# Kernel tuning notes

Hardware: AMD Instinct MI355X
Metric: run time of the kernel (lower is better)

## Reference

```python
import jax, jax.numpy as jnp
import numpy as np

B, T, V, D = 64, 2048, 32000, 256  # batch, seq_len, vocab, emb_dim == hidden_size
H = D
NUM_CLASSES = 27
N_NODES = 128


def setup_inputs() -> dict:
    key = jax.random.key(0)
    ks = jax.random.split(key, 8)
    s = 1.0 / np.sqrt(D)
    return {
        "tokens": jax.random.randint(ks[0], (B, T), 0, V),
        "node_token_span_starts": jax.random.randint(ks[1], (B, N_NODES), 0, T),
        "node_token_span_ends": jax.random.randint(ks[2], (B, N_NODES), 0, T),
        "embed": jax.random.normal(ks[3], (V, D), dtype=jnp.float32),
        "Wi": jax.random.normal(ks[4], (D, 4 * H), dtype=jnp.float32) * s,
        "Wh": jax.random.normal(ks[5], (H, 4 * H), dtype=jnp.float32) * s,
        "bh": jnp.zeros((4 * H,), dtype=jnp.float32),
        "Wo": jax.random.normal(ks[6], (H, NUM_CLASSES), dtype=jnp.float32) * s,
        "bo": jnp.zeros((NUM_CLASSES,), dtype=jnp.float32),
    }


def reference(tokens, node_token_span_starts, node_token_span_ends,
              embed, Wi, Wh, bh, Wo, bo):
    # node_token_span_* are unused by the original forward (dead code).
    x = embed[tokens.astype(jnp.int32)]            # [B, T, D]
    # Precompute input projections for all timesteps in one big GEMM.
    zx = jnp.einsum('btd,df->btf', x, Wi) + bh     # [B, T, 4H]
    batch = tokens.shape[0]
    c0 = jnp.zeros((batch, H), dtype=x.dtype)
    h0 = jnp.zeros((batch, H), dtype=x.dtype)

    def step(carry, zxt):
        c, h = carry
        z = zxt + h @ Wh                           # [B, 4H]
        i, f, g, o = jnp.split(z, 4, axis=-1)
        c = jax.nn.sigmoid(f) * c + jax.nn.sigmoid(i) * jnp.tanh(g)
        h = jax.nn.sigmoid(o) * jnp.tanh(c)
        return (c, h), h

    (c, h), _ = jax.lax.scan(step, (c0, h0), jnp.swapaxes(zx, 0, 1))
    # forward_outputs[:, -1, :] == final hidden state h
    return h @ Wo + bo                             # [B, NUM_CLASSES]
```

## Files before the change

### kernel.cpp

```cpp
#include <hip/hip_runtime.h>
#include <hip/hip_bf16.h>
#include <stdint.h>

typedef __hip_bfloat16 bf16;
typedef __attribute__((ext_vector_type(8))) short short8;
typedef __attribute__((ext_vector_type(4))) float f32x4;
typedef __attribute__((ext_vector_type(4))) int i32x4;
typedef __attribute__((ext_vector_type(4))) unsigned int u32x4;

#define NB   64
#define NT   2048
#define NV   32000
#define ND   256
#define NH4  1024
#define NCLS 27
#define CH   256
#define NCH  (NT / CH)


__global__ __launch_bounds__(256) void k_cvt_embed(const float* __restrict__ e,
                                                   bf16* __restrict__ o) {
  int i = blockIdx.x * blockDim.x + threadIdx.x;
  float4 v = reinterpret_cast<const float4*>(e)[i];
  union { bf16 h[4]; uint2 u; } pk;
  pk.h[0] = __float2bfloat16(v.x);
  pk.h[1] = __float2bfloat16(v.y);
  pk.h[2] = __float2bfloat16(v.z);
  pk.h[3] = __float2bfloat16(v.w);
  reinterpret_cast<uint2*>(o)[i] = pk.u;
}

__global__ __launch_bounds__(256) void k_cvt_wi(const float* __restrict__ wi,
                                                bf16* __restrict__ wit) {
  int i = blockIdx.x * blockDim.x + threadIdx.x;
  int col = i >> 8;
  int k   = i & 255;
  wit[i] = __float2bfloat16(wi[k * NH4 + col]);
}

__global__ __launch_bounds__(256) void k_scale(const float* __restrict__ wh,
                                               float* __restrict__ dq,
                                               float* __restrict__ rdq,
                                               float* __restrict__ rw) {
  int col = blockIdx.x * 256 + threadIdx.x;
  float m = 0.f;
  for (int k = 0; k < ND; ++k) m = fmaxf(m, fabsf(wh[k * NH4 + col]));
  dq[col]  = m * (1.f / 16129.f);
  rdq[col] = 16129.f / m;
  rw[col]  = 127.f / m;
}

__global__ __launch_bounds__(256) void k_cvt_whq(const float* __restrict__ wh,
                                                 const float* __restrict__ rw,
                                                 signed char* __restrict__ whq) {
  int idx  = blockIdx.x * 256 + threadIdx.x;
  int ii   = idx & 15;
  int lane = (idx >> 4) & 63;
  int kq   = (idx >> 10) & 3;
  int nt   = idx >> 12;
  int k   = kq * 64 + (lane >> 4) * 16 + ii;
  int col = nt * 16 + (lane & 15);
  whq[idx] = (signed char)(int)rintf(wh[k * NH4 + col] * rw[col]);
}

__device__ __forceinline__ float sigf(float x) {
  return __builtin_amdgcn_rcpf(1.f + __expf(-x));
}
__device__ __forceinline__ float tanh_fast(float x) {
  return 1.f - 2.f * __builtin_amdgcn_rcpf(1.f + __expf(2.f * x));
}

#define LSTM_STEP(ZX, ST)                                                       \
  {                                                                             \
    i32x4 a0 = *(const i32x4*)&aF[0 * 1024 + l * 16];                           \
    i32x4 a1 = *(const i32x4*)&aF[1 * 1024 + l * 16];                           \
    i32x4 a2 = *(const i32x4*)&aF[2 * 1024 + l * 16];                           \
    i32x4 a3 = *(const i32x4*)&aF[3 * 1024 + l * 16];                           \
    i32x4 acc[8];                                                               \
    _Pragma("unroll")                                                           \
    for (int j = 0; j < 8; ++j) {                                               \
      i32x4 t;                                                                  \
      t = __builtin_amdgcn_mfma_i32_16x16x64_i8(a0, w[j][0], czero, 0, 0, 0);   \
      t = __builtin_amdgcn_mfma_i32_16x16x64_i8(a1, w[j][1], t, 0, 0, 0);       \
      t = __builtin_amdgcn_mfma_i32_16x16x64_i8(a2, w[j][2], t, 0, 0, 0);       \
      acc[j] = __builtin_amdgcn_mfma_i32_16x16x64_i8(a3, w[j][3], t, 0, 0, 0);  \
    }                                                                           \
    if (l4 == 0) {                                                              \
      _Pragma("unroll")                                                         \
      for (int j = 0; j < 8; ++j) {                                             \
        int col = (wv * 8 + j) * 16 + l15;                                      \
        int tt  = ((col & 255) << 2) | (col >> 8);                              \
        zl[tt]        = acc[j][0];                                              \
        zl[1024 + tt] = acc[j][1];                                              \
      }                                                                         \
    }                                                                           \
    __syncthreads();                                                            \
    {                                                                           \
      i32x4 zr = *(const i32x4*)&zl[b * 1024 + u * 4];                          \
      int s0 = zr[0] + ZX[0];                                                   \
      int s1 = zr[1] + ZX[1];                                                   \
      int s2 = zr[2] + ZX[2];                                                   \
      int s3 = zr[3] + ZX[3];                                                   \
      if ((ST) + 2 < CH)                                                        \
        ZX = *(const i32x4*)(zg + (size_t)((ST) + 2) * 2048);                   \
      float zi = (float)s0 * dqv[0] + bhv[0];                                   \
      float zf = (float)s1 * dqv[1] + bhv[1];                                   \
      float zg_ = (float)s2 * dqv[2] + bhv[2];                                  \
      float zo = (float)s3 * dqv[3] + bhv[3];                                   \
      c = sigf(zf) * c + sigf(zi) * tanh_fast(zg_);                             \
      float h = sigf(zo) * tanh_fast(c);                                        \
      aF[kqu * 1024 + (b | (lgu << 4)) * 16 + iiu] =                            \
          (signed char)(int)rintf(h * 127.f);                                   \
      if ((ST) == CH - 1) hst[(p * 2 + b) * 256 + u] = h;                       \
    }                                                                           \
    __syncthreads();                                                            \
  }

__global__ __launch_bounds__(512, 1) void k_fused(const int*  __restrict__ tokens,
                                                  const bf16* __restrict__ eb,
                                                  const bf16* __restrict__ wit,
                                                  const float* __restrict__ rdq,
                                                  const signed char* __restrict__ whq,
                                                  const float* __restrict__ dq,
                                                  const float* __restrict__ bh,
                                                  float* __restrict__ cst,
                                                  float* __restrict__ hst,
                                                  int* __restrict__ zxqA,
                                                  int* __restrict__ zxqB,
                                                  int L) {
  __shared__ char smem[16384];
  int bid = blockIdx.x;

  if (bid < 32) {
    if (L == 0) return;
    int* zl = (int*)smem;
    signed char* aF = (signed char*)(smem + 8192);
    const int* __restrict__ zxq = ((L - 1) & 1) ? zxqB : zxqA;
    int t0 = (L - 1) * CH;

    int p   = bid;
    int tid = threadIdx.x;
    int l   = tid & 63;
    int wv  = tid >> 6;
    int l15 = l & 15, l4 = l >> 4;
    int u   = tid & 255;
    int b   = tid >> 8;

    i32x4 w[8][4];
#pragma unroll
    for (int j = 0; j < 8; ++j) {
      int nt = wv * 8 + j;
#pragma unroll
      for (int kq = 0; kq < 4; ++kq)
        w[j][kq] = *(const i32x4*)&whq[((nt * 4 + kq) * 64 + l) * 16];
    }
#pragma unroll
    for (int j = 0; j < 8; ++j)
#pragma unroll
      for (int kq = 0; kq < 4; ++kq)
        asm volatile("" : "+v"(w[j][kq]));

    i32x4 czero = (i32x4)0;
    asm volatile("" : "+v"(czero));

    float dqv[4], bhv[4];
#pragma unroll
    for (int q = 0; q < 4; ++q) { dqv[q] = dq[q * 256 + u]; bhv[q] = bh[q * 256 + u]; }
    float c = (t0 == 0) ? 0.f : cst[(p * 2 + b) * 256 + u];

    int kqu = u >> 6, lgu = (u >> 4) & 3, iiu = u & 15;

    if (tid < 256) ((i32x4*)aF)[tid] = (i32x4)0;
    __syncthreads();
    if (t0 != 0) {
      int hq = (int)rintf(hst[(p * 2 + b) * 256 + u] * 127.f);
      aF[kqu * 1024 + (b | (lgu << 4)) * 16 + iiu] = (signed char)hq;
    }
    __syncthreads();

    const int* zg = zxq + ((size_t)(p * CH) * 2 + b) * 1024 + u * 4;
    i32x4 zxA = *(const i32x4*)zg;
    i32x4 zxB = *(const i32x4*)(zg + 2048);

    for (int lt = 0; lt < CH; lt += 2) {
      LSTM_STEP(zxA, lt)
      LSTM_STEP(zxB, lt + 1)
    }

    cst[(p * 2 + b) * 256 + u] = c;

  } else {
    if (L >= NCH) return;
    int* __restrict__ zxw = (L & 1) ? zxqB : zxqA;
    int t0 = L * CH;
    int hh   = threadIdx.x >> 8;
    int tid2 = threadIdx.x & 255;
    bf16* As = (bf16*)(smem + hh * 8192);
    bf16* Bs = (bf16*)(smem + hh * 8192 + 4096);

    int lane = tid2 & 63, wave = tid2 >> 6;
    int wm   = wave >> 1, wn = wave & 1;
    int srow = tid2 >> 2;
    int skg  = tid2 & 3;
    bf16* as_dst = &As[(skg * 64 + srow) * 8];
    bf16* bs_dst = &Bs[(skg * 64 + srow) * 8];

    for (int it = 0; it < 16; ++it) {
      int tg = ((bid - 32) + it * 128) * 2 + hh;
      int mb = tg >> 4;
      int nb = tg & 15;
      int n0 = nb * 64;

      long trow = (long)tokens[srow * NT + t0 + mb] * ND;
      const bf16* ap = eb  + trow + skg * 8;
      const bf16* bp = wit + (long)(n0 + srow) * ND + skg * 8;

      f32x4 acc[2][2] = {};
      for (int k0 = 0; k0 < ND; k0 += 32) {
        __syncthreads();
        *(u32x4*)as_dst = *(const u32x4*)(ap + k0);
        *(u32x4*)bs_dst = *(const u32x4*)(bp + k0);
        __syncthreads();
        short8 a0 = *(const short8*)&As[((lane >> 4) * 64 + wm * 32 +  0 + (lane & 15)) * 8];
        short8 a1 = *(const short8*)&As[((lane >> 4) * 64 + wm * 32 + 16 + (lane & 15)) * 8];
        short8 b0 = *(const short8*)&Bs[((lane >> 4) * 64 + wn * 32 +  0 + (lane & 15)) * 8];
        short8 b1 = *(const short8*)&Bs[((lane >> 4) * 64 + wn * 32 + 16 + (lane & 15)) * 8];
        acc[0][0] = __builtin_amdgcn_mfma_f32_16x16x32_bf16(a0, b0, acc[0][0], 0, 0, 0);
        acc[0][1] = __builtin_amdgcn_mfma_f32_16x16x32_bf16(a0, b1, acc[0][1], 0, 0, 0);
        acc[1][0] = __builtin_amdgcn_mfma_f32_16x16x32_bf16(a1, b0, acc[1][0], 0, 0, 0);
        acc[1][1] = __builtin_amdgcn_mfma_f32_16x16x32_bf16(a1, b1, acc[1][1], 0, 0, 0);
      }

      int cb  = n0 + wn * 32 + (lane & 15);
      float rq0 = rdq[cb], rq1 = rdq[cb + 16];
      int bb = wm * 32 + (lane >> 4) * 4;
#pragma unroll
      for (int fm = 0; fm < 2; ++fm) {
#pragma unroll
        for (int fn = 0; fn < 2; ++fn) {
          int col = cb + fn * 16;
          int uu  = col & 255, q = col >> 8;
          float rq = fn ? rq1 : rq0;
#pragma unroll
          for (int i2 = 0; i2 < 4; ++i2) {
            int rr = bb + fm * 16 + i2;
            int p0 = rr >> 1;
            size_t idx = (((size_t)(p0 * CH) + mb) * 2 + (rr & 1)) * 1024 + uu * 4 + q;
            zxw[idx] = (int)rintf(acc[fm][fn][i2] * rq);
          }
        }
      }
    }
  }
}

__global__ __launch_bounds__(64) void k_out(const float* __restrict__ hfin,
                                            const float* __restrict__ wo,
                                            const float* __restrict__ bo,
                                            float* __restrict__ y) {
  __shared__ float hsm[256];
  int b = blockIdx.x, tid = threadIdx.x;
  for (int i = tid; i < 256; i += 64) hsm[i] = hfin[b * 256 + i];
  __syncthreads();
  if (tid < NCLS) {
    float s = bo[tid];
    for (int k = 0; k < 256; ++k) s += hsm[k] * wo[k * NCLS + tid];
    y[b * NCLS + tid] = s;
  }
}

extern "C" void kernel_launch(void* const* d_in, const int* in_sizes, int n_in,
                              void* d_out, int out_size, void* d_ws, size_t ws_size,
                              hipStream_t stream) {
  const int*   tokens = (const int*)d_in[0];
  const float* embed  = (const float*)d_in[3];
  const float* wi     = (const float*)d_in[4];
  const float* wh     = (const float*)d_in[5];
  const float* bh     = (const float*)d_in[6];
  const float* wo     = (const float*)d_in[7];
  const float* bo     = (const float*)d_in[8];
  float* y = (float*)d_out;

  char* ws = (char*)d_ws;
  bf16* eb         = (bf16*)ws;        ws += (size_t)NV * ND * 2;
  bf16* wit        = (bf16*)ws;        ws += (size_t)NH4 * ND * 2;
  signed char* whq = (signed char*)ws; ws += (size_t)ND * NH4;
  float* dqv       = (float*)ws;       ws += (size_t)NH4 * 4;
  float* rdq       = (float*)ws;       ws += (size_t)NH4 * 4;
  float* rw        = (float*)ws;       ws += (size_t)NH4 * 4;
  float* cst       = (float*)ws;       ws += (size_t)NB * ND * 4;
  float* hst       = (float*)ws;       ws += (size_t)NB * ND * 4;
  int* zxqA        = (int*)ws;         ws += (size_t)CH * 262144;
  int* zxqB        = (int*)ws;         ws += (size_t)CH * 262144;

  hipLaunchKernelGGL(k_cvt_embed, dim3(NV * ND / 4 / 256), dim3(256), 0, stream, embed, eb);
  hipLaunchKernelGGL(k_cvt_wi,    dim3(NH4 * ND / 256), dim3(256), 0, stream, wi, wit);
  hipLaunchKernelGGL(k_scale,     dim3(4), dim3(256), 0, stream, wh, dqv, rdq, rw);
  hipLaunchKernelGGL(k_cvt_whq,   dim3(1024), dim3(256), 0, stream, wh, rw, whq);

  for (int L = 0; L <= NCH; ++L) {
    hipLaunchKernelGGL(k_fused, dim3(160), dim3(512), 0, stream,
                       tokens, eb, wit, rdq, whq, dqv, bh, cst, hst,
                       zxqA, zxqB, L);
  }
  hipLaunchKernelGGL(k_out, dim3(NB), dim3(64), 0, stream, hst, wo, bo, y);
}
```

Baseline: 2.161 ms.

## Compute LSTM gates directly from MFMA accumulators with double-buffered h

Remaps the recurrent weight tiles so each wave's MFMA outputs hold all four gates for the same hidden units, so gate math runs in registers on the accumulator lanes. This removes the shared-memory z staging buffer and one of the two barriers per timestep, and double-buffers the quantized h fragment. The cost is that only a quarter of the lanes (l4==0) do the nonlinearities, four units each, which concentrates transcendental work on fewer threads.

```diff
diff --git a/kernel.cpp b/kernel.cpp
--- a/kernel.cpp
+++ b/kernel.cpp
@@ -70,50 +70,53 @@
   return 1.f - 2.f * __builtin_amdgcn_rcpf(1.f + __expf(2.f * x));
 }
 
-#define LSTM_STEP(ZX, ST)                                                       \
-  {                                                                             \
-    i32x4 a0 = *(const i32x4*)&aF[0 * 1024 + l * 16];                           \
-    i32x4 a1 = *(const i32x4*)&aF[1 * 1024 + l * 16];                           \
-    i32x4 a2 = *(const i32x4*)&aF[2 * 1024 + l * 16];                           \
-    i32x4 a3 = *(const i32x4*)&aF[3 * 1024 + l * 16];                           \
-    i32x4 acc[8];                                                               \
-    _Pragma("unroll")                                                           \
-    for (int j = 0; j < 8; ++j) {                                               \
-      i32x4 t;                                                                  \
-      t = __builtin_amdgcn_mfma_i32_16x16x64_i8(a0, w[j][0], czero, 0, 0, 0);   \
-      t = __builtin_amdgcn_mfma_i32_16x16x64_i8(a1, w[j][1], t, 0, 0, 0);       \
-      t = __builtin_amdgcn_mfma_i32_16x16x64_i8(a2, w[j][2], t, 0, 0, 0);       \
-      acc[j] = __builtin_amdgcn_mfma_i32_16x16x64_i8(a3, w[j][3], t, 0, 0, 0);  \
-    }                                                                           \
-    if (l4 == 0) {                                                              \
-      _Pragma("unroll")                                                         \
-      for (int j = 0; j < 8; ++j) {                                             \
-        int col = (wv * 8 + j) * 16 + l15;                                      \
-        int tt  = ((col & 255) << 2) | (col >> 8);                              \
-        zl[tt]        = acc[j][0];                                              \
-        zl[1024 + tt] = acc[j][1];                                              \
-      }                                                                         \
-    }                                                                           \
-    __syncthreads();                                                            \
-    {                                                                           \
-      i32x4 zr = *(const i32x4*)&zl[b * 1024 + u * 4];                          \
-      int s0 = zr[0] + ZX[0];                                                   \
-      int s1 = zr[1] + ZX[1];                                                   \
-      int s2 = zr[2] + ZX[2];                                                   \
-      int s3 = zr[3] + ZX[3];                                                   \
-      if ((ST) + 2 < CH)                                                        \
-        ZX = *(const i32x4*)(zg + (size_t)((ST) + 2) * 2048);                   \
-      float zi = (float)s0 * dqv[0] + bhv[0];                                   \
-      float zf = (float)s1 * dqv[1] + bhv[1];                                   \
-      float zg_ = (float)s2 * dqv[2] + bhv[2];                                  \
-      float zo = (float)s3 * dqv[3] + bhv[3];                                   \
-      c = sigf(zf) * c + sigf(zi) * tanh_fast(zg_);                             \
-      float h = sigf(zo) * tanh_fast(c);                                        \
-      aF[kqu * 1024 + (b | (lgu << 4)) * 16 + iiu] =                            \
-          (signed char)(int)rintf(h * 127.f);                                   \
-      if ((ST) == CH - 1) hst[(p * 2 + b) * 256 + u] = h;                       \
-    }                                                                           \
-    __syncthreads();                                                            \
+#define LSTM_STEP(ZX, AR, AW, ST)                                              \
+  {                                                                            \
+    i32x4 a0 = *(const i32x4*)&AR[0 * 1024 + l * 16];                          \
+    i32x4 a1 = *(const i32x4*)&AR[1 * 1024 + l * 16];                          \
+    i32x4 a2 = *(const i32x4*)&AR[2 * 1024 + l * 16];                          \
+    i32x4 a3 = *(const i32x4*)&AR[3 * 1024 + l * 16];                          \
+    i32x4 acc[8];                                                              \
+    _Pragma("unroll")                                                          \
+    for (int j = 0; j < 8; ++j) {                                              \
+      i32x4 t;                                                                 \
+      t = __builtin_amdgcn_mfma_i32_16x16x64_i8(a0, w[j][0], czero, 0, 0, 0);  \
+      t = __builtin_amdgcn_mfma_i32_16x16x64_i8(a1, w[j][1], t, 0, 0, 0);      \
+      t = __builtin_amdgcn_mfma_i32_16x16x64_i8(a2, w[j][2], t, 0, 0, 0);      \
+      acc[j] = __builtin_amdgcn_mfma_i32_16x16x64_i8(a3, w[j][3], t, 0, 0, 0); \
+    }                                                                          \
+    if (l4 == 0) {                                                             \
+      _Pragma("unroll")                                                        \
+      for (int gs = 0; gs < 2; ++gs) {                                         \
+        _Pragma("unroll")                                                      \
+        for (int bb = 0; bb < 2; ++bb) {                                       \
+          int s0 = acc[0 * 2 + gs][bb] + ZX[bb * 2 + gs][0];                   \
+          int s1 = acc[1 * 2 + gs][bb] + ZX[bb * 2 + gs][1];                   \
+          int s2 = acc[2 * 2 + gs][bb] + ZX[bb * 2 + gs][2];                   \
+          int s3 = acc[3 * 2 + gs][bb] + ZX[bb * 2 + gs][3];                   \
+          float zi  = (float)s0 * dqv[gs][0] + bhv[gs][0];                     \
+          float zf  = (float)s1 * dqv[gs][1] + bhv[gs][1];                     \
+          float zg_ = (float)s2 * dqv[gs][2] + bhv[gs][2];                     \
+          float zo  = (float)s3 * dqv[gs][3] + bhv[gs][3];                     \
+          int cc = gs * 2 + bb;                                                \
+          c[cc] = sigf(zf) * c[cc] + sigf(zi) * tanh_fast(zg_);                \
+          float hv = sigf(zo) * tanh_fast(c[cc]);                              \
+          AW[(gs ? kq1 : kq0) * 1024 + (bb + 16 * (gs ? lg1 : lg0)) * 16 + l] =\
+              (signed char)(int)rintf(hv * 127.f);                             \
+          if ((ST) == CH - 1) hst[(p * 2 + bb) * 256 + (gs ? u1 : u0)] = hv;   \
+        }                                                                      \
+      }                                                                        \
+      if ((ST) + 2 < CH) {                                                     \
+        const int* zn = zg + (size_t)((ST) + 2) * 2048;                        \
+        _Pragma("unroll")                                                      \
+        for (int gs = 0; gs < 2; ++gs)                                         \
+          _Pragma("unroll")                                                    \
+          for (int bb = 0; bb < 2; ++bb)                                       \
+            ZX[bb * 2 + gs] =                                                  \
+                *(const i32x4*)(zn + bb * 1024 + (gs ? u1 : u0) * 4);          \
+      }                                                                        \
+    }                                                                          \
+    __syncthreads();                                                           \
   }
 
 __global__ __launch_bounds__(512, 1) void k_fused(const int*  __restrict__ tokens,
@@ -133,8 +136,8 @@
 
   if (bid < 32) {
     if (L == 0) return;
-    int* zl = (int*)smem;
-    signed char* aF = (signed char*)(smem + 8192);
+    signed char* aF0 = (signed char*)smem;
+    signed char* aF1 = (signed char*)(smem + 4096);
     const int* __restrict__ zxq = ((L - 1) & 1) ? zxqB : zxqA;
     int t0 = (L - 1) * CH;
 
@@ -142,14 +145,12 @@
     int tid = threadIdx.x;
     int l   = tid & 63;
     int wv  = tid >> 6;
-    int l15 = l & 15, l4 = l >> 4;
-    int u   = tid & 255;
-    int b   = tid >> 8;
+    int l4  = l >> 4;
 
     i32x4 w[8][4];
 #pragma unroll
     for (int j = 0; j < 8; ++j) {
-      int nt = wv * 8 + j;
+      int nt = (j >> 1) * 16 + wv + 8 * (j & 1);
 #pragma unroll
       for (int kq = 0; kq < 4; ++kq)
         w[j][kq] = *(const i32x4*)&whq[((nt * 4 + kq) * 64 + l) * 16];
@@ -163,31 +164,64 @@
     i32x4 czero = (i32x4)0;
     asm volatile("" : "+v"(czero));
 
-    float dqv[4], bhv[4];
-#pragma unroll
-    for (int q = 0; q < 4; ++q) { dqv[q] = dq[q * 256 + u]; bhv[q] = bh[q * 256 + u]; }
-    float c = (t0 == 0) ? 0.f : cst[(p * 2 + b) * 256 + u];
-
-    int kqu = u >> 6, lgu = (u >> 4) & 3, iiu = u & 15;
-
-    if (tid < 256) ((i32x4*)aF)[tid] = (i32x4)0;
+    int ll = l & 15;
+    int u0 = wv * 16 + ll;
+    int u1 = (wv + 8) * 16 + ll;
+    float dqv[2][4], bhv[2][4];
+#pragma unroll
+    for (int q = 0; q < 4; ++q) {
+      dqv[0][q] = dq[q * 256 + u0]; bhv[0][q] = bh[q * 256 + u0];
+      dqv[1][q] = dq[q * 256 + u1]; bhv[1][q] = bh[q * 256 + u1];
+    }
+    int kq0 = u0 >> 6, lg0 = (u0 >> 4) & 3;
+    int kq1 = u1 >> 6, lg1 = (u1 >> 4) & 3;
+
+    float c[4];
+#pragma unroll
+    for (int gs = 0; gs < 2; ++gs)
+#pragma unroll
+      for (int bb = 0; bb < 2; ++bb)
+        c[gs * 2 + bb] = (t0 == 0) ? 0.f
+                       : cst[(p * 2 + bb) * 256 + (gs ? u1 : u0)];
+
+    ((i32x4*)smem)[tid] = (i32x4)0;
     __syncthreads();
-    if (t0 != 0) {
-      int hq = (int)rintf(hst[(p * 2 + b) * 256 + u] * 127.f);
-      aF[kqu * 1024 + (b | (lgu << 4)) * 16 + iiu] = (signed char)hq;
+    if (t0 != 0 && l4 == 0) {
+#pragma unroll
+      for (int gs = 0; gs < 2; ++gs)
+#pragma unroll
+        for (int bb = 0; bb < 2; ++bb) {
+          float hv = hst[(p * 2 + bb) * 256 + (gs ? u1 : u0)];
+          aF0[(gs ? kq1 : kq0) * 1024 + (bb + 16 * (gs ? lg1 : lg0)) * 16 + l] =
+              (signed char)(int)rintf(hv * 127.f);
+        }
     }
     __syncthreads();
 
-    const int* zg = zxq + ((size_t)(p * CH) * 2 + b) * 1024 + u * 4;
-    i32x4 zxA = *(const i32x4*)zg;
-    i32x4 zxB = *(const i32x4*)(zg + 2048);
+    const int* zg = zxq + (size_t)(p * CH) * 2048;
+    i32x4 zxA[4], zxB[4];
+    if (l4 == 0) {
+#pragma unroll
+      for (int gs = 0; gs < 2; ++gs)
+#pragma unroll
+        for (int bb = 0; bb < 2; ++bb) {
+          zxA[bb * 2 + gs] = *(const i32x4*)(zg + bb * 1024 + (gs ? u1 : u0) * 4);
+          zxB[bb * 2 + gs] = *(const i32x4*)(zg + 2048 + bb * 1024 + (gs ? u1 : u0) * 4);
+        }
+    }
 
     for (int lt = 0; lt < CH; lt += 2) {
-      LSTM_STEP(zxA, lt)
-      LSTM_STEP(zxB, lt + 1)
-    }
-
-    cst[(p * 2 + b) * 256 + u] = c;
+      LSTM_STEP(zxA, aF0, aF1, lt)
+      LSTM_STEP(zxB, aF1, aF0, lt + 1)
+    }
+
+    if (l4 == 0) {
+#pragma unroll
+      for (int gs = 0; gs < 2; ++gs)
+#pragma unroll
+        for (int bb = 0; bb < 2; ++bb)
+          cst[(p * 2 + bb) * 256 + (gs ? u1 : u0)] = c[gs * 2 + bb];
+    }
 
   } else {
     if (L >= NCH) return;
```

After: 2.738 ms. 1.27x slower.
